# Kernel tuning notes

Measured on AMD Instinct MI355X. Metric: run time of the kernel, lower is better.

## Reference

```python
import jax, jax.numpy as jnp
import numpy as np

D_MODEL = 4096
D_FIBER = 16
D_CONTROL = 64
EMA_MOMENTUM = 0.9


def setup_inputs() -> dict:
    key = jax.random.key(0)
    k_h, k_f, k_w1, k_w2 = jax.random.split(key, 4)
    B, S = 4, 2048
    hidden = jax.random.normal(k_h, (B, S, D_MODEL), dtype=jnp.float32)
    # torch nn.Linear stores weight as [out, in]; fiber_proj init: normal std=0.02
    W_fiber = jax.random.normal(k_f, (D_FIBER, D_MODEL), dtype=jnp.float32) * 0.02
    # predictor[0]: Linear(d_model+d_fiber, d_control) with default torch init (uniform)
    fan_in1 = D_MODEL + D_FIBER
    bound1 = 1.0 / np.sqrt(fan_in1)
    W1 = jax.random.uniform(k_w1, (D_CONTROL, fan_in1), dtype=jnp.float32, minval=-bound1, maxval=bound1)
    b1 = jnp.zeros((D_CONTROL,), dtype=jnp.float32)
    # predictor[-2]: Linear(d_control, 1), weight normal std=0.01, bias zero
    W2 = jax.random.normal(k_w2, (1, D_CONTROL), dtype=jnp.float32) * 0.01
    b2 = jnp.zeros((1,), dtype=jnp.float32)
    lam = jnp.asarray(1.0, dtype=jnp.float32)
    return {"hidden": hidden, "W_fiber": W_fiber, "W1": W1, "b1": b1, "W2": W2, "b2": b2, "lam": lam}


def _causal_ema(delta_h, alpha):
    # h_t = alpha*h_{t-1} + (1-alpha)*d_t, h_{-1} = 0. delta_h: [B,S]
    B = delta_h.shape[0]
    def step(h_prev, d_t):
        h_t = alpha * h_prev + (1.0 - alpha) * d_t
        return h_t, h_t
    _, hs = jax.lax.scan(step, jnp.zeros((B,), delta_h.dtype), jnp.swapaxes(delta_h, 0, 1))
    return jnp.swapaxes(hs, 0, 1)  # [B,S]


def reference(hidden, W_fiber, W1, b1, W2, b2, lam):
    h = hidden.astype(jnp.float32)                      # [B,S,D]
    fiber = jnp.einsum('bsd,fd->bsf', h, W_fiber)       # [B,S,16]
    combined = jnp.concatenate([h, fiber], axis=-1)     # [B,S,D+16]
    z = jax.nn.gelu(jnp.einsum('bsc,kc->bsk', combined, W1) + b1, approximate=False)
    delta_h = jax.nn.softplus(jnp.einsum('bsk,ok->bso', z, W2) + b2)[..., 0]  # [B,S]
    field = _causal_ema(delta_h, EMA_MOMENTUM)          # [B,S]
    gate = jax.nn.sigmoid(-lam * field)
    return gate.astype(hidden.dtype), field.astype(hidden.dtype), delta_h.mean()
```

## Files before the change

### kernel.cpp

```cpp
#include <hip/hip_runtime.h>
#include <hip/hip_bf16.h>

#define D_MODEL 4096
#define NTOK    8192
#define SEQ     2048

typedef short bf16x8 __attribute__((ext_vector_type(8)));
typedef float f32x4  __attribute__((ext_vector_type(4)));

__device__ inline short f2bf(float x) {
  __hip_bfloat16 h = __float2bfloat16(x);
  return *reinterpret_cast<short*>(&h);
}
__device__ inline float bf2f(const void* p, size_t i) {
  return __bfloat162float(((const __hip_bfloat16*)p)[i]);
}

__global__ __launch_bounds__(320) void sniff_k(const void* hid, const void* wf,
                                               const void* w1, const void* w2,
                                               const void* b1, const void* b2,
                                               const void* lam,
                                               int* flags, float* scal) {
  int wv = threadIdx.x >> 6, lane = threadIdx.x & 63;
  const unsigned short* p = nullptr;
  int n = 0;
  switch (wv) {
    case 0: p = (const unsigned short*)hid; n = NTOK * D_MODEL; break;
    case 1: p = (const unsigned short*)wf;  n = 16 * D_MODEL;   break;
    case 2: p = (const unsigned short*)w1;  n = 64 * 4112;      break;
    case 3: p = (const unsigned short*)w2;  n = 64;             break;
    case 4: p = (const unsigned short*)b1;  n = 64;             break;
  }
  int S = n / 2 < 64 ? n / 2 : 64;
  bool act = lane < S;
  unsigned short ve = 0, vo = 0;
  if (act) { ve = p[2 * lane]; vo = p[2 * lane + 1]; }
  int ee = (ve >> 7) & 0xFF, eo = (vo >> 7) & 0xFF;
  bool ve_band   = (ve == 0) || (ve == 0x8000) || (ee >= 96 && ee <= 141);
  bool vo_bandnz = (vo != 0) && (vo != 0x8000) && (eo >= 96 && eo <= 141);
  int zp = __popcll(__ballot(act && ve == 0 && vo == 0));
  int ob = __popcll(__ballot(act && ve == 0 && vo_bandnz));
  int eb = __popcll(__ballot(act && ve_band));
  if (lane == 0) {
    int f;
    if (zp == S) f = 1;
    else if (4 * ob >= 3 * S) f = 0;
    else if (4 * eb >= 3 * S) f = 1;
    else f = 0;
    flags[wv] = f;
  }
  if (threadIdx.x == 0) {
    unsigned short l0 = *(const unsigned short*)lam;
    int le = (l0 >> 7) & 0xFF;
    if (l0 != 0 && l0 != 0x8000 && le >= 96 && le <= 141)
      scal[0] = __bfloat162float(*(const __hip_bfloat16*)lam);
    else
      scal[0] = *(const float*)lam;
    unsigned short c0 = *(const unsigned short*)b2;
    int ce = (c0 >> 7) & 0xFF;
    if (c0 == 0) scal[1] = 0.0f;
    else if (c0 != 0x8000 && ce >= 96 && ce <= 141)
      scal[1] = __bfloat162float(*(const __hip_bfloat16*)b2);
    else
      scal[1] = *(const float*)b2;
  }
}

__global__ __launch_bounds__(256) void fold_w1(const void* __restrict__ W1v,
                                               const void* __restrict__ Wfv,
                                               const int* __restrict__ flags,
                                               __hip_bfloat16* __restrict__ W1eff) {
  int n = blockIdx.x;
  int fw1 = flags[2], fwf = flags[1];
  __shared__ float w1b[16];
  if (threadIdx.x < 16) {
    size_t idx = (size_t)n * 4112 + 4096 + threadIdx.x;
    w1b[threadIdx.x] = fw1 ? bf2f(W1v, idx) : ((const float*)W1v)[idx];
  }
  __syncthreads();
  for (int k = threadIdx.x; k < D_MODEL; k += 256) {
    size_t idx = (size_t)n * 4112 + k;
    float v = fw1 ? bf2f(W1v, idx) : ((const float*)W1v)[idx];
#pragma unroll
    for (int f = 0; f < 16; ++f) {
      size_t wi = (size_t)f * D_MODEL + k;
      float wfv = fwf ? bf2f(Wfv, wi) : ((const float*)Wfv)[wi];
      v += w1b[f] * wfv;
    }
    W1eff[(size_t)n * D_MODEL + k] = __float2bfloat16(v);
  }
}

__global__ __launch_bounds__(512, 4) void gemm_delta(const void* __restrict__ hid,
                                                     const short* __restrict__ B_,
                                                     const void* __restrict__ b1,
                                                     const void* __restrict__ w2,
                                                     const int* __restrict__ flags,
                                                     const float* __restrict__ scal,
                                                     float* __restrict__ delta) {
  int tile = blockIdx.x;
  int w    = threadIdx.x >> 6;
  int lane = threadIdx.x & 63;
  int m = lane & 15, kg = lane >> 4;
  size_t abase = (size_t)(tile * 16 + m) * D_MODEL + w * 512 + kg * 8;
  const short* Bp = B_ + (size_t)m * D_MODEL + w * 512 + kg * 8;
  f32x4 acc0 = {0.f, 0.f, 0.f, 0.f};
  f32x4 acc1 = acc0, acc2 = acc0, acc3 = acc0;
  if (flags[0]) {
    const short* Ap = (const short*)hid + abase;
    bf16x8 areg[8];
#pragma unroll
    for (int s = 0; s < 8; ++s) areg[s] = *(const bf16x8*)(Ap + s * 32);
#pragma unroll
    for (int s = 0; s < 16; ++s) {
      bf16x8 a = areg[s & 7];
      if (s + 8 < 16) areg[s & 7] = *(const bf16x8*)(Ap + (s + 8) * 32);
      bf16x8 b0  = *(const bf16x8*)(Bp + s * 32);
      bf16x8 b1f = *(const bf16x8*)(Bp + 16 * D_MODEL + s * 32);
      bf16x8 b2f = *(const bf16x8*)(Bp + 32 * D_MODEL + s * 32);
      bf16x8 b3f = *(const bf16x8*)(Bp + 48 * D_MODEL + s * 32);
      acc0 = __builtin_amdgcn_mfma_f32_16x16x32_bf16(a, b0, acc0, 0, 0, 0);
      acc1 = __builtin_amdgcn_mfma_f32_16x16x32_bf16(a, b1f, acc1, 0, 0, 0);
      acc2 = __builtin_amdgcn_mfma_f32_16x16x32_bf16(a, b2f, acc2, 0, 0, 0);
      acc3 = __builtin_amdgcn_mfma_f32_16x16x32_bf16(a, b3f, acc3, 0, 0, 0);
    }
  } else {
    const float* Ap = (const float*)hid + abase;
#pragma unroll 2
    for (int ks = 0; ks < 512; ks += 32) {
      float4 lo = *(const float4*)(Ap + ks);
      float4 hi = *(const float4*)(Ap + ks + 4);
      bf16x8 a;
      a[0] = f2bf(lo.x); a[1] = f2bf(lo.y); a[2] = f2bf(lo.z); a[3] = f2bf(lo.w);
      a[4] = f2bf(hi.x); a[5] = f2bf(hi.y); a[6] = f2bf(hi.z); a[7] = f2bf(hi.w);
      bf16x8 b0  = *(const bf16x8*)(Bp + ks);
      bf16x8 b1f = *(const bf16x8*)(Bp + 16 * D_MODEL + ks);
      bf16x8 b2f = *(const bf16x8*)(Bp + 32 * D_MODEL + ks);
      bf16x8 b3f = *(const bf16x8*)(Bp + 48 * D_MODEL + ks);
      acc0 = __builtin_amdgcn_mfma_f32_16x16x32_bf16(a, b0, acc0, 0, 0, 0);
      acc1 = __builtin_amdgcn_mfma_f32_16x16x32_bf16(a, b1f, acc1, 0, 0, 0);
      acc2 = __builtin_amdgcn_mfma_f32_16x16x32_bf16(a, b2f, acc2, 0, 0, 0);
      acc3 = __builtin_amdgcn_mfma_f32_16x16x32_bf16(a, b3f, acc3, 0, 0, 0);
    }
  }
  __shared__ float red[8][16][64];
#pragma unroll
  for (int r = 0; r < 4; ++r) {
    int row = kg * 4 + r;
    red[w][row][ 0 + m] = acc0[r];
    red[w][row][16 + m] = acc1[r];
    red[w][row][32 + m] = acc2[r];
    red[w][row][48 + m] = acc3[r];
  }
  __syncthreads();
  int row = threadIdx.x >> 5, cid = threadIdx.x & 31;
  int fb1 = flags[4], fw2 = flags[3];
  float y = 0.f;
#pragma unroll
  for (int j = 0; j < 2; ++j) {
    int c = cid + 32 * j;
    float s = 0.f;
#pragma unroll
    for (int ch = 0; ch < 8; ++ch) s += red[ch][row][c];
    s += fb1 ? bf2f(b1, c) : ((const float*)b1)[c];
    float g = 0.5f * s * (1.0f + erff(s * 0.70710678118654752f));
    y += g * (fw2 ? bf2f(w2, c) : ((const float*)w2)[c]);
  }
#pragma unroll
  for (int off = 1; off <= 16; off <<= 1) y += __shfl_xor(y, off, 64);
  if (cid == 0) {
    float x = y + scal[1];
    float d = (x > 20.0f) ? x : log1pf(expf(x));
    delta[tile * 16 + row] = d;
  }
}

__global__ __launch_bounds__(256) void ema_out(const float* __restrict__ delta,
                                               const float* __restrict__ scal,
                                               float* __restrict__ out) {
  int b    = threadIdx.x >> 6;
  int lane = threadIdx.x & 63;
  const float alpha = 0.9f;
  float d[32];
  const float* dp = delta + b * SEQ + lane * 32;
  float beta = 0.f, lsum = 0.f;
#pragma unroll
  for (int i = 0; i < 32; ++i) {
    d[i] = dp[i];
    lsum += d[i];
    beta = alpha * beta + 0.1f * d[i];
  }
  float accA = 0.03433683820292512f;
  float accB = beta;
  for (int off = 1; off < 64; off <<= 1) {
    float uA = __shfl_up(accA, off, 64);
    float uB = __shfl_up(accB, off, 64);
    if (lane >= off) {
      accB = accB + accA * uB;
      accA = accA * uA;
    }
  }
  float prev = __shfl_up(accB, 1, 64);
  float h = (lane == 0) ? 0.f : prev;
  float lam = scal[0];
#pragma unroll
  for (int i = 0; i < 32; ++i) {
    h = alpha * h + 0.1f * d[i];
    float gate = 1.0f / (1.0f + expf(lam * h));
    out[b * SEQ + lane * 32 + i]        = gate;
    out[NTOK + b * SEQ + lane * 32 + i] = h;
  }
#pragma unroll
  for (int off = 32; off >= 1; off >>= 1) lsum += __shfl_xor(lsum, off, 64);
  __shared__ float bs[4];
  if (lane == 0) bs[b] = lsum;
  __syncthreads();
  if (threadIdx.x == 0)
    out[2 * NTOK] = (bs[0] + bs[1] + bs[2] + bs[3]) * (1.0f / 8192.0f);
}

extern "C" void kernel_launch(void* const* d_in, const int* in_sizes, int n_in,
                              void* d_out, int out_size, void* d_ws, size_t ws_size,
                              hipStream_t stream) {
  const void* hidden = d_in[0];
  const void* Wf     = d_in[1];
  const void* W1     = d_in[2];
  const void* b1     = d_in[3];
  const void* W2     = d_in[4];
  const void* b2     = d_in[5];
  const void* lam    = d_in[6];
  float* out = (float*)d_out;

  char* ws = (char*)d_ws;
  int*   flags = (int*)ws;
  float* scal  = (float*)(ws + 32);
  __hip_bfloat16* W1eff = (__hip_bfloat16*)(ws + 64);
  float* delta = (float*)(ws + 64 + (size_t)64 * D_MODEL * 2);

  sniff_k<<<1, 320, 0, stream>>>(hidden, Wf, W1, W2, b1, b2, lam, flags, scal);
  fold_w1<<<64, 256, 0, stream>>>(W1, Wf, flags, W1eff);
  gemm_delta<<<512, 512, 0, stream>>>(hidden, (const short*)W1eff, b1, W2, flags, scal, delta);
  ema_out<<<1, 256, 0, stream>>>(delta, scal, out);
}
```

Measured before the change: 247.3 us.

## Split K across blocks with LDS-staged W1 slice and separate epilogue kernel

The GEMM is repartitioned so each block owns one 512-wide K chunk and 128 tokens. It stages the 64x512 W1eff slice once into swizzled shared memory and reuses it across 8 waves, where before each wave read B from global or L2. Per-chunk fp32 partial sums go to a workspace buffer, and a new epilogue kernel reduces the 8 chunks and applies bias, GELU, the W2 dot and softplus. This cuts redundant B traffic, but adds an extra kernel launch and a 16 MB partial-sum write and read-back.

```diff
diff --git a/kernel.cpp b/kernel.cpp
--- a/kernel.cpp
+++ b/kernel.cpp
@@ -91,87 +91,114 @@
   }
 }
 
-__global__ __launch_bounds__(512, 4) void gemm_delta(const void* __restrict__ hid,
-                                                     const short* __restrict__ B_,
-                                                     const void* __restrict__ b1,
-                                                     const void* __restrict__ w2,
-                                                     const int* __restrict__ flags,
-                                                     const float* __restrict__ scal,
-                                                     float* __restrict__ delta) {
-  int tile = blockIdx.x;
+__global__ __launch_bounds__(512, 4) void gemm_part(const void* __restrict__ hid,
+                                                    const short* __restrict__ B_,
+                                                    const int* __restrict__ flags,
+                                                    float* __restrict__ part) {
+  int c = blockIdx.x >> 6;
+  int t = blockIdx.x & 63;
   int w    = threadIdx.x >> 6;
   int lane = threadIdx.x & 63;
   int m = lane & 15, kg = lane >> 4;
-  size_t abase = (size_t)(tile * 16 + m) * D_MODEL + w * 512 + kg * 8;
-  const short* Bp = B_ + (size_t)m * D_MODEL + w * 512 + kg * 8;
+
+  __shared__ short Bs[64 * 512];
+
+#pragma unroll
+  for (int i = 0; i < 8; ++i) {
+    int n    = (threadIdx.x >> 6) + i * 8;
+    int kb16 = threadIdx.x & 63;
+    bf16x8 v = *(const bf16x8*)(B_ + (size_t)n * D_MODEL + c * 512 + kb16 * 8);
+    *(bf16x8*)(Bs + kb16 * 512 + ((n ^ (kb16 & 7)) * 8)) = v;
+  }
+  __syncthreads();
+
   f32x4 acc0 = {0.f, 0.f, 0.f, 0.f};
   f32x4 acc1 = acc0, acc2 = acc0, acc3 = acc0;
+  size_t abase = (size_t)(t * 128 + w * 16 + m) * D_MODEL + c * 512 + kg * 8;
   if (flags[0]) {
     const short* Ap = (const short*)hid + abase;
     bf16x8 areg[8];
 #pragma unroll
-    for (int s = 0; s < 8; ++s) areg[s] = *(const bf16x8*)(Ap + s * 32);
+    for (int i = 0; i < 8; ++i) areg[i] = *(const bf16x8*)(Ap + i * 32);
 #pragma unroll
     for (int s = 0; s < 16; ++s) {
       bf16x8 a = areg[s & 7];
       if (s + 8 < 16) areg[s & 7] = *(const bf16x8*)(Ap + (s + 8) * 32);
-      bf16x8 b0  = *(const bf16x8*)(Bp + s * 32);
-      bf16x8 b1f = *(const bf16x8*)(Bp + 16 * D_MODEL + s * 32);
-      bf16x8 b2f = *(const bf16x8*)(Bp + 32 * D_MODEL + s * 32);
-      bf16x8 b3f = *(const bf16x8*)(Bp + 48 * D_MODEL + s * 32);
+      int kb16 = s * 4 + kg;
+      int swz  = (kb16 & 7);
+      const short* bp = Bs + kb16 * 512;
+      bf16x8 b0 = *(const bf16x8*)(bp + (((m +  0) ^ swz) * 8));
+      bf16x8 b1 = *(const bf16x8*)(bp + (((m + 16) ^ swz) * 8));
+      bf16x8 b2 = *(const bf16x8*)(bp + (((m + 32) ^ swz) * 8));
+      bf16x8 b3 = *(const bf16x8*)(bp + (((m + 48) ^ swz) * 8));
       acc0 = __builtin_amdgcn_mfma_f32_16x16x32_bf16(a, b0, acc0, 0, 0, 0);
-      acc1 = __builtin_amdgcn_mfma_f32_16x16x32_bf16(a, b1f, acc1, 0, 0, 0);
-      acc2 = __builtin_amdgcn_mfma_f32_16x16x32_bf16(a, b2f, acc2, 0, 0, 0);
-      acc3 = __builtin_amdgcn_mfma_f32_16x16x32_bf16(a, b3f, acc3, 0, 0, 0);
+      acc1 = __builtin_amdgcn_mfma_f32_16x16x32_bf16(a, b1, acc1, 0, 0, 0);
+      acc2 = __builtin_amdgcn_mfma_f32_16x16x32_bf16(a, b2, acc2, 0, 0, 0);
+      acc3 = __builtin_amdgcn_mfma_f32_16x16x32_bf16(a, b3, acc3, 0, 0, 0);
     }
   } else {
     const float* Ap = (const float*)hid + abase;
-#pragma unroll 2
-    for (int ks = 0; ks < 512; ks += 32) {
-      float4 lo = *(const float4*)(Ap + ks);
-      float4 hi = *(const float4*)(Ap + ks + 4);
+#pragma unroll 4
+    for (int s = 0; s < 16; ++s) {
+      float4 lo = *(const float4*)(Ap + s * 32);
+      float4 hi = *(const float4*)(Ap + s * 32 + 4);
       bf16x8 a;
       a[0] = f2bf(lo.x); a[1] = f2bf(lo.y); a[2] = f2bf(lo.z); a[3] = f2bf(lo.w);
       a[4] = f2bf(hi.x); a[5] = f2bf(hi.y); a[6] = f2bf(hi.z); a[7] = f2bf(hi.w);
-      bf16x8 b0  = *(const bf16x8*)(Bp + ks);
-      bf16x8 b1f = *(const bf16x8*)(Bp + 16 * D_MODEL + ks);
-      bf16x8 b2f = *(const bf16x8*)(Bp + 32 * D_MODEL + ks);
-      bf16x8 b3f = *(const bf16x8*)(Bp + 48 * D_MODEL + ks);
+      int kb16 = s * 4 + kg;
+      int swz  = (kb16 & 7);
+      const short* bp = Bs + kb16 * 512;
+      bf16x8 b0 = *(const bf16x8*)(bp + (((m +  0) ^ swz) * 8));
+      bf16x8 b1 = *(const bf16x8*)(bp + (((m + 16) ^ swz) * 8));
+      bf16x8 b2 = *(const bf16x8*)(bp + (((m + 32) ^ swz) * 8));
+      bf16x8 b3 = *(const bf16x8*)(bp + (((m + 48) ^ swz) * 8));
       acc0 = __builtin_amdgcn_mfma_f32_16x16x32_bf16(a, b0, acc0, 0, 0, 0);
-      acc1 = __builtin_amdgcn_mfma_f32_16x16x32_bf16(a, b1f, acc1, 0, 0, 0);
-      acc2 = __builtin_amdgcn_mfma_f32_16x16x32_bf16(a, b2f, acc2, 0, 0, 0);
-      acc3 = __builtin_amdgcn_mfma_f32_16x16x32_bf16(a, b3f, acc3, 0, 0, 0);
-    }
-  }
-  __shared__ float red[8][16][64];
+      acc1 = __builtin_amdgcn_mfma_f32_16x16x32_bf16(a, b1, acc1, 0, 0, 0);
+      acc2 = __builtin_amdgcn_mfma_f32_16x16x32_bf16(a, b2, acc2, 0, 0, 0);
+      acc3 = __builtin_amdgcn_mfma_f32_16x16x32_bf16(a, b3, acc3, 0, 0, 0);
+    }
+  }
+
+  float* po = part + ((size_t)c * NTOK + (size_t)t * 128 + w * 16) * 64;
 #pragma unroll
   for (int r = 0; r < 4; ++r) {
     int row = kg * 4 + r;
-    red[w][row][ 0 + m] = acc0[r];
-    red[w][row][16 + m] = acc1[r];
-    red[w][row][32 + m] = acc2[r];
-    red[w][row][48 + m] = acc3[r];
-  }
-  __syncthreads();
-  int row = threadIdx.x >> 5, cid = threadIdx.x & 31;
+    po[row * 64 + (m +  0)] = acc0[r];
+    po[row * 64 + (m + 16)] = acc1[r];
+    po[row * 64 + (m + 32)] = acc2[r];
+    po[row * 64 + (m + 48)] = acc3[r];
+  }
+}
+
+__global__ __launch_bounds__(256) void delta_ep(const float* __restrict__ part,
+                                                const void* __restrict__ b1,
+                                                const void* __restrict__ w2,
+                                                const int* __restrict__ flags,
+                                                const float* __restrict__ scal,
+                                                float* __restrict__ delta) {
+  int t   = blockIdx.x & 63;
+  int sub = blockIdx.x >> 6;
+  int tok = t * 128 + sub * 16 + (threadIdx.x >> 4);
+  int cid = threadIdx.x & 15;
   int fb1 = flags[4], fw2 = flags[3];
   float y = 0.f;
 #pragma unroll
-  for (int j = 0; j < 2; ++j) {
-    int c = cid + 32 * j;
+  for (int j = 0; j < 4; ++j) {
+    int col = cid + 16 * j;
     float s = 0.f;
 #pragma unroll
-    for (int ch = 0; ch < 8; ++ch) s += red[ch][row][c];
-    s += fb1 ? bf2f(b1, c) : ((const float*)b1)[c];
+    for (int c = 0; c < 8; ++c)
+      s += part[((size_t)c * NTOK + tok) * 64 + col];
+    s += fb1 ? bf2f(b1, col) : ((const float*)b1)[col];
     float g = 0.5f * s * (1.0f + erff(s * 0.70710678118654752f));
-    y += g * (fw2 ? bf2f(w2, c) : ((const float*)w2)[c]);
-  }
-#pragma unroll
-  for (int off = 1; off <= 16; off <<= 1) y += __shfl_xor(y, off, 64);
+    y += g * (fw2 ? bf2f(w2, col) : ((const float*)w2)[col]);
+  }
+#pragma unroll
+  for (int off = 1; off <= 8; off <<= 1) y += __shfl_xor(y, off, 64);
   if (cid == 0) {
     float x = y + scal[1];
     float d = (x > 20.0f) ? x : log1pf(expf(x));
-    delta[tile * 16 + row] = d;
+    delta[tok] = d;
   }
 }
 
@@ -236,9 +263,11 @@
   float* scal  = (float*)(ws + 32);
   __hip_bfloat16* W1eff = (__hip_bfloat16*)(ws + 64);
   float* delta = (float*)(ws + 64 + (size_t)64 * D_MODEL * 2);
+  float* part  = (float*)(ws + 64 + (size_t)64 * D_MODEL * 2 + NTOK * 4);
 
   sniff_k<<<1, 320, 0, stream>>>(hidden, Wf, W1, W2, b1, b2, lam, flags, scal);
   fold_w1<<<64, 256, 0, stream>>>(W1, Wf, flags, W1eff);
-  gemm_delta<<<512, 512, 0, stream>>>(hidden, (const short*)W1eff, b1, W2, flags, scal, delta);
+  gemm_part<<<512, 512, 0, stream>>>(hidden, (const short*)W1eff, flags, part);
+  delta_ep<<<512, 256, 0, stream>>>(part, b1, W2, flags, scal, delta);
   ema_out<<<1, 256, 0, stream>>>(delta, scal, out);
 }
```

Measured after the change: 238.6 us. 1.04x faster.
